# Kernel tuning notes

Hardware: AMD Instinct MI355X
Metric: run time of the kernel (lower is better)

The kernel has to match this reference:

```python
import jax, jax.numpy as jnp
import numpy as np

H = 768      # hidden_size
NH = 12      # num_heads
HD = H // NH # head_size
MLP = 3072
B, N = 16, 577


def setup_inputs() -> dict:
    key = jax.random.key(0)
    ks = jax.random.split(key, 16)
    s = 0.02
    return {
        "x": jax.random.normal(ks[0], (B, N, H), jnp.float32),
        "Wq": jax.random.normal(ks[1], (H, H), jnp.float32) * s,
        "bq": jnp.zeros((H,), jnp.float32),
        "Wk": jax.random.normal(ks[2], (H, H), jnp.float32) * s,
        "bk": jnp.zeros((H,), jnp.float32),
        "Wv": jax.random.normal(ks[3], (H, H), jnp.float32) * s,
        "bv": jnp.zeros((H,), jnp.float32),
        "Wo": jax.random.normal(ks[4], (H, H), jnp.float32) * s,
        "bo": jnp.zeros((H,), jnp.float32),
        "W1": jax.random.normal(ks[5], (H, MLP), jnp.float32) * s,
        "b1": jnp.zeros((MLP,), jnp.float32),
        "W2": jax.random.normal(ks[6], (MLP, H), jnp.float32) * s,
        "b2": jnp.zeros((H,), jnp.float32),
        "ln1_g": jnp.ones((H,), jnp.float32),
        "ln1_b": jnp.zeros((H,), jnp.float32),
        "ln2_g": jnp.ones((H,), jnp.float32),
        "ln2_b": jnp.zeros((H,), jnp.float32),
    }


def _layernorm(x, g, b, eps=1e-6):
    mu = jnp.mean(x, axis=-1, keepdims=True)
    var = jnp.mean(jnp.square(x - mu), axis=-1, keepdims=True)
    return (x - mu) * jax.lax.rsqrt(var + eps) * g + b


def reference(x, Wq, bq, Wk, bk, Wv, bv, Wo, bo, W1, b1, W2, b2,
              ln1_g, ln1_b, ln2_g, ln2_b):
    h = x
    y = _layernorm(x, ln1_g, ln1_b)
    # projections [B,N,H] -> [B,NH,N,HD]
    def heads(t):
        return t.reshape(B, N, NH, HD).transpose(0, 2, 1, 3)
    q = heads(y @ Wq + bq)
    _k = heads(y @ Wk + bk)  # computed but UNUSED (bug in original: Q@V^T)
    v = heads(y @ Wv + bv)
    # faithful to source: scores = Q @ V^T (not K)
    scores = jnp.einsum('bhqd,bhkd->bhqk', q, v) / jnp.sqrt(jnp.float32(HD))
    probs = jax.nn.softmax(scores, axis=-1)
    o = jnp.einsum('bhqk,bhkd->bhqd', probs, v)
    o = o.transpose(0, 2, 1, 3).reshape(B, N, H)
    attn_out = o @ Wo + bo
    x1 = attn_out + h
    h2 = x1
    y2 = _layernorm(x1, ln2_g, ln2_b)
    m = jax.nn.gelu(y2 @ W1 + b1, approximate=False)
    m = m @ W2 + b2
    return m + h2
```

## Files before the change

### kernel.cpp

```cpp
#include <hip/hip_runtime.h>


#define GLOBAL_AS __attribute__((address_space(1)))
#define LDS_AS __attribute__((address_space(3)))

typedef __bf16 bf16x8 __attribute__((ext_vector_type(8)));
typedef float f32x4 __attribute__((ext_vector_type(4)));
typedef unsigned short u16x8 __attribute__((ext_vector_type(8)));

static __device__ __forceinline__ f32x4 mfma16(bf16x8 a, bf16x8 b, f32x4 c) {
  return __builtin_amdgcn_mfma_f32_16x16x32_bf16(a, b, c, 0, 0, 0);
}

static __device__ __forceinline__ unsigned short f2bf(float f) {
  union { float f; unsigned u; } v; v.f = f;
  unsigned r = v.u + 0x7fffu + ((v.u >> 16) & 1u);
  return (unsigned short)(r >> 16);
}

static __device__ __forceinline__ void async16(const void* g, void* l) {
  __builtin_amdgcn_global_load_lds((const GLOBAL_AS void*)g, (LDS_AS void*)l, 16, 0, 0);
}

static __device__ __forceinline__ float gelu_exact(float x) {
  return 0.5f * x * (1.0f + erff(x * 0.70710678118654752f));
}

static __device__ __forceinline__ void tc_body(const float* __restrict__ W,
                                               unsigned short* __restrict__ Wt,
                                               int K, int ldw, int nb, int kb,
                                               int t) {
  __shared__ float tile[32][33];
  const int tr = t >> 5, tc = t & 31;
#pragma unroll
  for (int p = 0; p < 4; ++p)
    tile[p * 8 + tr][tc] = W[(size_t)(kb + p * 8 + tr) * ldw + nb + tc];
  __syncthreads();
#pragma unroll
  for (int p = 0; p < 4; ++p)
    Wt[(size_t)(nb + p * 8 + tr) * K + kb + tc] = f2bf(tile[tc][p * 8 + tr]);
}

__global__ __launch_bounds__(256)
void transpose_all(const float* __restrict__ Wq, const float* __restrict__ Wv,
                   const float* __restrict__ Wo, const float* __restrict__ W1,
                   const float* __restrict__ W2, unsigned short* __restrict__ R3) {
  const size_t S = 589824;
  int id = blockIdx.x;
  const int t = threadIdx.x;
  if (id < 1728) {
    const float* W = id < 576 ? Wq : (id < 1152 ? Wv : Wo);
    unsigned short* dst = R3 + (size_t)(id / 576) * S;
    id %= 576;
    tc_body(W, dst, 768, 768, (id % 24) * 32, (id / 24) * 32, t);
  } else {
    id -= 1728;
    const int seg = id / 1152;
    id %= 1152;
    const int s = seg >> 1;
    if ((seg & 1) == 0) {
      unsigned short* dst = R3 + 3 * S + (size_t)s * 4 * S;
      tc_body(W1 + s * 1536, dst, 768, 3072, (id % 48) * 32, (id / 48) * 32, t);
    } else {
      unsigned short* dst = R3 + 5 * S + (size_t)s * 4 * S;
      tc_body(W2 + (size_t)s * 1536 * 768, dst, 1536, 768, (id % 24) * 32,
              (id / 24) * 32, t);
    }
  }
}

__global__ __launch_bounds__(256)
void ln_f32(const float* __restrict__ x, const float* __restrict__ g,
            const float* __restrict__ be, unsigned short* __restrict__ y) {
  const int w = threadIdx.x >> 6, lane = threadIdx.x & 63;
  const size_t row = (size_t)blockIdx.x * 4 + w;
  const float* xr = x + row * 768;
  float vv[12];
#pragma unroll
  for (int j = 0; j < 3; ++j) {
    float4 v = *(const float4*)(xr + j * 256 + lane * 4);
    vv[j * 4 + 0] = v.x; vv[j * 4 + 1] = v.y;
    vv[j * 4 + 2] = v.z; vv[j * 4 + 3] = v.w;
  }
  float s = 0.f;
#pragma unroll
  for (int j = 0; j < 12; ++j) s += vv[j];
#pragma unroll
  for (int o = 32; o > 0; o >>= 1) s += __shfl_xor(s, o);
  const float mu = s * (1.0f / 768.0f);
  float q = 0.f;
#pragma unroll
  for (int j = 0; j < 12; ++j) { float d = vv[j] - mu; q += d * d; }
#pragma unroll
  for (int o = 32; o > 0; o >>= 1) q += __shfl_xor(q, o);
  const float rstd = rsqrtf(q * (1.0f / 768.0f) + 1e-6f);
  unsigned short* yr = y + row * 768;
#pragma unroll
  for (int j = 0; j < 3; ++j) {
    float4 gv = *(const float4*)(g + j * 256 + lane * 4);
    float4 bv = *(const float4*)(be + j * 256 + lane * 4);
    ushort4 o4;
    o4.x = f2bf((vv[j * 4 + 0] - mu) * rstd * gv.x + bv.x);
    o4.y = f2bf((vv[j * 4 + 1] - mu) * rstd * gv.y + bv.y);
    o4.z = f2bf((vv[j * 4 + 2] - mu) * rstd * gv.z + bv.z);
    o4.w = f2bf((vv[j * 4 + 3] - mu) * rstd * gv.w + bv.w);
    *(ushort4*)(yr + j * 256 + lane * 4) = o4;
  }
}

template <int ACT, int RES, int OUTF32, int NB, int SPLIT>
__global__ __launch_bounds__(256, 2)
void gemm_bt(const unsigned short* __restrict__ A,
             const unsigned short* __restrict__ B,
             const float* __restrict__ bias,
             const float* __restrict__ bias2,
             const float* __restrict__ resid,
             void* __restrict__ out1, void* __restrict__ out2,
             int M, int N, int K) {
  __shared__ __align__(16) unsigned short As[3][128 * 32];
  __shared__ __align__(16) unsigned short Bs[3][128 * 32];
  const int t = threadIdx.x;
  const int nwg = gridDim.x;
  const int q8 = nwg >> 3, r8 = nwg & 7;
  const int xcd = blockIdx.x & 7, jj = blockIdx.x >> 3;
  const int wgid = (xcd < r8 ? xcd * (q8 + 1) : r8 * (q8 + 1) + (xcd - r8) * q8) + jj;
  const int gn = N >> 7;
  const int m0 = (wgid / gn) * 128;
  const int n0 = (wgid % gn) * 128;
  const int w = t >> 6, lane = t & 63;
  const int lr = lane & 15, lg = lane >> 4;
  const int wrr = (w >> 1) * 64, wcc = (w & 1) * 64;
  f32x4 acc[4][4] = {};

  auto stage = [&](int buf, int k0) {
#pragma unroll
    for (int p = 0; p < 2; ++p) {
      int i = p * 256 + t;
      int row = i >> 2, c = (i & 3) << 3;
      int ar = m0 + row; ar = ar < M ? ar : M - 1;
      async16(A + (size_t)ar * K + k0 + c, &As[buf][i * 8]);
      async16(B + (size_t)(n0 + row) * K + k0 + c, &Bs[buf][i * 8]);
    }
  };

  stage(0, 0);
  stage(1, 32);
  const int nt = K >> 5;
  int cur = 0, nx = 2;
  for (int tt = 0; tt < nt; ++tt) {
    if (tt + 1 < nt)
      asm volatile("s_waitcnt vmcnt(4)" ::: "memory");
    else
      asm volatile("s_waitcnt vmcnt(0)" ::: "memory");
    __builtin_amdgcn_s_barrier();
    __builtin_amdgcn_sched_barrier(0);
    if (tt + 2 < nt) stage(nx, (tt + 2) << 5);
    bf16x8 af[4], bfr[4];
#pragma unroll
    for (int mi = 0; mi < 4; ++mi)
      af[mi] = *(const bf16x8*)(&As[cur][(wrr + mi * 16 + lr) * 32 + lg * 8]);
#pragma unroll
    for (int ni = 0; ni < 4; ++ni)
      bfr[ni] = *(const bf16x8*)(&Bs[cur][(wcc + ni * 16 + lr) * 32 + lg * 8]);
    asm volatile("s_waitcnt lgkmcnt(0)" ::: "memory");
    __builtin_amdgcn_sched_barrier(0);
    __builtin_amdgcn_s_setprio(1);
#pragma unroll
    for (int mi = 0; mi < 4; ++mi)
#pragma unroll
      for (int ni = 0; ni < 4; ++ni)
        acc[mi][ni] = mfma16(af[mi], bfr[ni], acc[mi][ni]);
    __builtin_amdgcn_s_setprio(0);
    cur = (cur == 2) ? 0 : cur + 1;
    nx = (nx == 2) ? 0 : nx + 1;
  }
  const int orow = m0 + wrr + lg * 4;
  const int ocol = n0 + wcc + lr;
#pragma unroll
  for (int mi = 0; mi < 4; ++mi) {
#pragma unroll
    for (int ni = 0; ni < 4; ++ni) {
      const int col = ocol + ni * 16;
      float bs;
      if (SPLIT)
        bs = (col < 768) ? bias[col] : bias2[col - 768];
      else
        bs = NB ? 0.f : bias[col];
      f32x4 a = acc[mi][ni];
#pragma unroll
      for (int r = 0; r < 4; ++r) {
        const int row = orow + mi * 16 + r;
        if (row < M) {
          float v = a[r] + bs;
          if (ACT == 1) v = gelu_exact(v);
          if (RES == 1) v += resid[(size_t)row * N + col];
          if (SPLIT) {
            if (col < 768)
              ((unsigned short*)out1)[(size_t)row * 768 + col] = f2bf(v);
            else
              ((unsigned short*)out2)[(size_t)row * 768 + col - 768] = f2bf(v);
          } else if (OUTF32) {
            ((float*)out1)[(size_t)row * N + col] = v;
          } else {
            ((unsigned short*)out1)[(size_t)row * N + col] = f2bf(v);
          }
        }
      }
    }
  }
}

__global__ __launch_bounds__(256, 2)
void attn_fused(const unsigned short* __restrict__ Q,
                const unsigned short* __restrict__ V,
                unsigned short* __restrict__ O) {
  __shared__ __align__(16) unsigned short Vn[64 * 72];
  __shared__ __align__(16) unsigned short Vt[64 * 72];
  __shared__ __align__(16) unsigned short Pl[4][32 * 72];
  const int qt = blockIdx.x, h = blockIdx.y, b = blockIdx.z;
  const int t = threadIdx.x, w = t >> 6, lane = t & 63;
  const int lr = lane & 15, lg = lane >> 4;
  const int q0 = qt * 128 + w * 32;
  bf16x8 aq[2][2];
#pragma unroll
  for (int mi = 0; mi < 2; ++mi) {
    int qrow = q0 + mi * 16 + lr; qrow = qrow < 577 ? qrow : 576;
    const unsigned short* qp = Q + ((size_t)(b * 577 + qrow)) * 768 + h * 64;
    aq[mi][0] = *(const bf16x8*)(qp + lg * 8);
    aq[mi][1] = *(const bf16x8*)(qp + 32 + lg * 8);
  }
  bf16x8 ones;
#pragma unroll
  for (int j = 0; j < 8; ++j) ones[j] = (__bf16)1.0f;
  f32x4 oacc[2][4] = {};
  f32x4 lac[2] = {};
  const unsigned short* vp = V + (size_t)b * 577 * 768 + h * 64;

  for (int kt = 0; kt < 10; ++kt) {
    const int k0 = kt * 64;
#pragma unroll
    for (int p = 0; p < 2; ++p) {
      int i = p * 256 + t;
      int kr = i >> 3, c = (i & 7) << 3;
      int gk = k0 + kr; gk = gk < 577 ? gk : 576;
      bf16x8 vv = *(const bf16x8*)(vp + (size_t)gk * 768 + c);
      *(bf16x8*)(Vn + kr * 72 + c) = vv;
    }
    __syncthreads();
#pragma unroll
    for (int p = 0; p < 2; ++p) {
      int i = p * 256 + t;
      int d = i & 63, kb = (i >> 6) * 8;
      u16x8 tv;
#pragma unroll
      for (int j = 0; j < 8; ++j) tv[j] = Vn[(kb + j) * 72 + d];
      *(u16x8*)(Vt + d * 72 + kb) = tv;
    }
    f32x4 s[2][4];
#pragma unroll
    for (int mi = 0; mi < 2; ++mi)
#pragma unroll
      for (int ni = 0; ni < 4; ++ni) {
        f32x4 a = {};
        a = mfma16(aq[mi][0], *(const bf16x8*)(Vn + (ni * 16 + lr) * 72 + lg * 8), a);
        a = mfma16(aq[mi][1], *(const bf16x8*)(Vn + (ni * 16 + lr) * 72 + 32 + lg * 8), a);
        s[mi][ni] = a * 0.125f;
      }
    if (kt == 9) {
#pragma unroll
      for (int ni = 0; ni < 4; ++ni) {
        int kc = k0 + ni * 16 + lr;
        if (kc >= 577) {
#pragma unroll
          for (int mi = 0; mi < 2; ++mi) {
            s[mi][ni][0] = -1e30f; s[mi][ni][1] = -1e30f;
            s[mi][ni][2] = -1e30f; s[mi][ni][3] = -1e30f;
          }
        }
      }
    }
#pragma unroll
    for (int mi = 0; mi < 2; ++mi)
#pragma unroll
      for (int ni = 0; ni < 4; ++ni)
#pragma unroll
        for (int r = 0; r < 4; ++r)
          Pl[w][(mi * 16 + lg * 4 + r) * 72 + ni * 16 + lr] =
              f2bf(__expf(s[mi][ni][r]));
    __syncthreads();
#pragma unroll
    for (int mi = 0; mi < 2; ++mi) {
      const bf16x8 pa0 = *(const bf16x8*)(&Pl[w][(mi * 16 + lr) * 72 + lg * 8]);
      const bf16x8 pa1 = *(const bf16x8*)(&Pl[w][(mi * 16 + lr) * 72 + 32 + lg * 8]);
#pragma unroll
      for (int di = 0; di < 4; ++di) {
        oacc[mi][di] = mfma16(pa0, *(const bf16x8*)(Vt + (di * 16 + lr) * 72 + lg * 8), oacc[mi][di]);
        oacc[mi][di] = mfma16(pa1, *(const bf16x8*)(Vt + (di * 16 + lr) * 72 + 32 + lg * 8), oacc[mi][di]);
      }
      lac[mi] = mfma16(pa0, ones, lac[mi]);
      lac[mi] = mfma16(pa1, ones, lac[mi]);
    }
  }
#pragma unroll
  for (int mi = 0; mi < 2; ++mi)
#pragma unroll
    for (int r = 0; r < 4; ++r) {
      const int qg = q0 + mi * 16 + lg * 4 + r;
      if (qg < 577) {
        const float inv = 1.0f / lac[mi][r];
        unsigned short* op = O + ((size_t)(b * 577 + qg)) * 768 + h * 64 + lr;
#pragma unroll
        for (int di = 0; di < 4; ++di) op[di * 16] = f2bf(oacc[mi][di][r] * inv);
      }
    }
}

extern "C" void kernel_launch(void* const* d_in, const int* in_sizes, int n_in,
                              void* d_out, int out_size, void* d_ws, size_t ws_size,
                              hipStream_t stream) {
  (void)in_sizes; (void)n_in; (void)out_size; (void)ws_size;
  const float* x   = (const float*)d_in[0];
  const float* Wq  = (const float*)d_in[1];
  const float* bq  = (const float*)d_in[2];
  const float* Wv  = (const float*)d_in[5];
  const float* bv  = (const float*)d_in[6];
  const float* Wo  = (const float*)d_in[7];
  const float* bo  = (const float*)d_in[8];
  const float* W1  = (const float*)d_in[9];
  const float* b1  = (const float*)d_in[10];
  const float* W2  = (const float*)d_in[11];
  const float* b2  = (const float*)d_in[12];
  const float* g1  = (const float*)d_in[13];
  const float* be1 = (const float*)d_in[14];
  const float* g2  = (const float*)d_in[15];
  const float* be2 = (const float*)d_in[16];
  float* out = (float*)d_out;

  const size_t BF = (size_t)9232 * 768 * 2;
  const size_t S = 589824;
  char* ws = (char*)d_ws;
  unsigned short* R0 = (unsigned short*)(ws);
  unsigned short* R1 = (unsigned short*)(ws + BF);
  unsigned short* R2 = (unsigned short*)(ws + 2 * BF);
  unsigned short* R3 = (unsigned short*)(ws + 3 * BF);
  unsigned short* WqT = R3;
  unsigned short* WoT = R3 + 2 * S;
  unsigned short* W1T0 = R3 + 3 * S;
  unsigned short* W2T0 = R3 + 5 * S;
  unsigned short* W1T1 = R3 + 7 * S;
  unsigned short* W2T1 = R3 + 9 * S;
  unsigned short* mb = R1;

  dim3 blk(256);

  transpose_all<<<dim3(6336), blk, 0, stream>>>(Wq, Wv, Wo, W1, W2, R3);

  ln_f32<<<dim3(2308), blk, 0, stream>>>(x, g1, be1, R0);

  gemm_bt<0, 0, 0, 0, 1><<<dim3(876), blk, 0, stream>>>(
      R0, WqT, bq, bv, nullptr, R1, R2, 9232, 1536, 768);

  attn_fused<<<dim3(5, 12, 16), blk, 0, stream>>>(R1, R2, R0);

  gemm_bt<0, 1, 1, 0, 0><<<dim3(438), blk, 0, stream>>>(
      R0, WoT, bo, nullptr, x, out, nullptr, 9232, 768, 768);

  ln_f32<<<dim3(2308), blk, 0, stream>>>(out, g2, be2, R0);

  gemm_bt<1, 0, 0, 0, 0><<<dim3(876), blk, 0, stream>>>(
      R0, W1T0, b1, nullptr, nullptr, mb, nullptr, 9232, 1536, 768);
  gemm_bt<0, 1, 1, 0, 0><<<dim3(438), blk, 0, stream>>>(
      mb, W2T0, b2, nullptr, out, out, nullptr, 9232, 768, 1536);
  gemm_bt<1, 0, 0, 0, 0><<<dim3(876), blk, 0, stream>>>(
      R0, W1T1, b1 + 1536, nullptr, nullptr, mb, nullptr, 9232, 1536, 768);
  gemm_bt<0, 1, 1, 1, 0><<<dim3(438), blk, 0, stream>>>(
      mb, W2T1, nullptr, nullptr, out, out, nullptr, 9232, 768, 1536);
}
```

Before: 405.1 us.

## Unroll GEMM main loop by three with static buffers and earlier prefetch issue

```diff
diff --git a/kernel.cpp b/kernel.cpp
--- a/kernel.cpp
+++ b/kernel.cpp
@@ -143,37 +143,44 @@
     }
   };
 
+#define GEMM_BODY(BUF, TT, MODE)                                              \
+  {                                                                           \
+    if (MODE == 0) {                                                          \
+      stage(((BUF) + 2) % 3, ((TT) + 2) << 5);                                \
+      asm volatile("s_waitcnt vmcnt(8)" ::: "memory");                        \
+    } else if (MODE == 1) {                                                   \
+      asm volatile("s_waitcnt vmcnt(4)" ::: "memory");                        \
+    } else {                                                                  \
+      asm volatile("s_waitcnt vmcnt(0)" ::: "memory");                        \
+    }                                                                         \
+    __builtin_amdgcn_s_barrier();         \
+    bf16x8 af[4], bfr[4];                                                     \
+    _Pragma("unroll") for (int mi = 0; mi < 4; ++mi) af[mi] =                 \
+        *(const bf16x8*)(&As[BUF][(wrr + mi * 16 + lr) * 32 + lg * 8]);       \
+    _Pragma("unroll") for (int ni = 0; ni < 4; ++ni) bfr[ni] =                \
+        *(const bf16x8*)(&Bs[BUF][(wcc + ni * 16 + lr) * 32 + lg * 8]);       \
+    asm volatile("s_waitcnt lgkmcnt(0)" ::: "memory");                        \
+    __builtin_amdgcn_sched_barrier(0);                          \
+    __builtin_amdgcn_s_barrier();          \
+    _Pragma("unroll") for (int mi = 0; mi < 4; ++mi)                          \
+        _Pragma("unroll") for (int ni = 0; ni < 4; ++ni) acc[mi][ni] =        \
+            mfma16(af[mi], bfr[ni], acc[mi][ni]);                             \
+  }
+
   stage(0, 0);
   stage(1, 32);
   const int nt = K >> 5;
-  int cur = 0, nx = 2;
-  for (int tt = 0; tt < nt; ++tt) {
-    if (tt + 1 < nt)
-      asm volatile("s_waitcnt vmcnt(4)" ::: "memory");
-    else
-      asm volatile("s_waitcnt vmcnt(0)" ::: "memory");
-    __builtin_amdgcn_s_barrier();
-    __builtin_amdgcn_sched_barrier(0);
-    if (tt + 2 < nt) stage(nx, (tt + 2) << 5);
-    bf16x8 af[4], bfr[4];
-#pragma unroll
-    for (int mi = 0; mi < 4; ++mi)
-      af[mi] = *(const bf16x8*)(&As[cur][(wrr + mi * 16 + lr) * 32 + lg * 8]);
-#pragma unroll
-    for (int ni = 0; ni < 4; ++ni)
-      bfr[ni] = *(const bf16x8*)(&Bs[cur][(wcc + ni * 16 + lr) * 32 + lg * 8]);
-    asm volatile("s_waitcnt lgkmcnt(0)" ::: "memory");
-    __builtin_amdgcn_sched_barrier(0);
-    __builtin_amdgcn_s_setprio(1);
-#pragma unroll
-    for (int mi = 0; mi < 4; ++mi)
-#pragma unroll
-      for (int ni = 0; ni < 4; ++ni)
-        acc[mi][ni] = mfma16(af[mi], bfr[ni], acc[mi][ni]);
-    __builtin_amdgcn_s_setprio(0);
-    cur = (cur == 2) ? 0 : cur + 1;
-    nx = (nx == 2) ? 0 : nx + 1;
-  }
+  int tt = 0;
+  for (; tt < nt - 3; tt += 3) {
+    GEMM_BODY(0, tt, 0);
+    GEMM_BODY(1, tt + 1, 0);
+    GEMM_BODY(2, tt + 2, 0);
+  }
+  GEMM_BODY(0, tt, 0);
+  GEMM_BODY(1, tt + 1, 1);
+  GEMM_BODY(2, tt + 2, 2);
+#undef GEMM_BODY
+
   const int orow = m0 + wrr + lg * 4;
   const int ocol = n0 + wcc + lr;
 #pragma unroll
```

After: 357.8 us. -11.7%, faster.

## Switch GEMM to double-buffered BK=64 tiles with XOR-swizzled LDS layout

Applied to the files above, without the earlier changes.

```diff
diff --git a/kernel.cpp b/kernel.cpp
--- a/kernel.cpp
+++ b/kernel.cpp
@@ -117,8 +117,8 @@
              const float* __restrict__ resid,
              void* __restrict__ out1, void* __restrict__ out2,
              int M, int N, int K) {
-  __shared__ __align__(16) unsigned short As[3][128 * 32];
-  __shared__ __align__(16) unsigned short Bs[3][128 * 32];
+  __shared__ __align__(16) unsigned short As[2][128 * 64];
+  __shared__ __align__(16) unsigned short Bs[2][128 * 64];
   const int t = threadIdx.x;
   const int nwg = gridDim.x;
   const int q8 = nwg >> 3, r8 = nwg & 7;
@@ -134,45 +134,56 @@
 
   auto stage = [&](int buf, int k0) {
 #pragma unroll
-    for (int p = 0; p < 2; ++p) {
+    for (int p = 0; p < 4; ++p) {
       int i = p * 256 + t;
-      int row = i >> 2, c = (i & 3) << 3;
+      int row = i >> 3;
+      int c = ((i ^ row) & 7) << 3;
       int ar = m0 + row; ar = ar < M ? ar : M - 1;
       async16(A + (size_t)ar * K + k0 + c, &As[buf][i * 8]);
+    }
+#pragma unroll
+    for (int p = 0; p < 4; ++p) {
+      int i = p * 256 + t;
+      int row = i >> 3;
+      int c = ((i ^ row) & 7) << 3;
       async16(B + (size_t)(n0 + row) * K + k0 + c, &Bs[buf][i * 8]);
     }
   };
 
   stage(0, 0);
-  stage(1, 32);
-  const int nt = K >> 5;
-  int cur = 0, nx = 2;
+  int cur = 0;
+  const int nt = K >> 6;
   for (int tt = 0; tt < nt; ++tt) {
-    if (tt + 1 < nt)
-      asm volatile("s_waitcnt vmcnt(4)" ::: "memory");
-    else
+    if (tt + 1 < nt) {
+      stage(cur ^ 1, (tt + 1) << 6);
+      asm volatile("s_waitcnt vmcnt(8)" ::: "memory");
+    } else {
       asm volatile("s_waitcnt vmcnt(0)" ::: "memory");
+    }
     __builtin_amdgcn_s_barrier();
-    __builtin_amdgcn_sched_barrier(0);
-    if (tt + 2 < nt) stage(nx, (tt + 2) << 5);
-    bf16x8 af[4], bfr[4];
-#pragma unroll
-    for (int mi = 0; mi < 4; ++mi)
-      af[mi] = *(const bf16x8*)(&As[cur][(wrr + mi * 16 + lr) * 32 + lg * 8]);
-#pragma unroll
-    for (int ni = 0; ni < 4; ++ni)
-      bfr[ni] = *(const bf16x8*)(&Bs[cur][(wcc + ni * 16 + lr) * 32 + lg * 8]);
+    bf16x8 af[2][4], bfr[2][4];
+#pragma unroll
+    for (int kk = 0; kk < 2; ++kk) {
+#pragma unroll
+      for (int mi = 0; mi < 4; ++mi)
+        af[kk][mi] = *(const bf16x8*)(
+            &As[cur][(wrr + mi * 16 + lr) * 64 + (((kk << 2) | lg) ^ (lr & 7)) * 8]);
+#pragma unroll
+      for (int ni = 0; ni < 4; ++ni)
+        bfr[kk][ni] = *(const bf16x8*)(
+            &Bs[cur][(wcc + ni * 16 + lr) * 64 + (((kk << 2) | lg) ^ (lr & 7)) * 8]);
+    }
     asm volatile("s_waitcnt lgkmcnt(0)" ::: "memory");
     __builtin_amdgcn_sched_barrier(0);
-    __builtin_amdgcn_s_setprio(1);
-#pragma unroll
-    for (int mi = 0; mi < 4; ++mi)
-#pragma unroll
-      for (int ni = 0; ni < 4; ++ni)
-        acc[mi][ni] = mfma16(af[mi], bfr[ni], acc[mi][ni]);
-    __builtin_amdgcn_s_setprio(0);
-    cur = (cur == 2) ? 0 : cur + 1;
-    nx = (nx == 2) ? 0 : nx + 1;
+    __builtin_amdgcn_s_barrier();
+#pragma unroll
+    for (int kk = 0; kk < 2; ++kk)
+#pragma unroll
+      for (int mi = 0; mi < 4; ++mi)
+#pragma unroll
+        for (int ni = 0; ni < 4; ++ni)
+          acc[mi][ni] = mfma16(af[kk][mi], bfr[kk][ni], acc[mi][ni]);
+    cur ^= 1;
   }
   const int orow = m0 + wrr + lg * 4;
   const int ocol = n0 + wcc + lr;
```

Result: faster. 352.2 us (-13.0%).
